# Kernel optimization log

Measured on AMD Instinct MI355X. Metric: run time of the kernel, lower is better.

Reference implementation:

```python
import jax, jax.numpy as jnp
import numpy as np

H = 10  # hidden_size


def _lstm_cell(x, h, c, Wih, Whh, bih, bhh):
    # PyTorch LSTMCell: gates ordered i, f, g, o
    gates = x @ Wih.T + bih + h @ Whh.T + bhh  # [B, 4H]
    i, f, g, o = jnp.split(gates, 4, axis=-1)
    c_new = jax.nn.sigmoid(f) * c + jax.nn.sigmoid(i) * jnp.tanh(g)
    h_new = jax.nn.sigmoid(o) * jnp.tanh(c_new)
    return h_new, c_new


def setup_inputs() -> dict:
    key = jax.random.key(0)
    ks = jax.random.split(key, 12)
    B, T = 16384, 2048
    s = 1.0 / np.sqrt(H)  # PyTorch LSTMCell init scale
    inp = {
        "x": jax.random.normal(ks[0], (B, T, 2), dtype=jnp.float32),
        "WihA": jax.random.uniform(ks[1], (4 * H, 2), minval=-s, maxval=s),
        "WhhA": jax.random.uniform(ks[2], (4 * H, H), minval=-s, maxval=s),
        "bihA": jax.random.uniform(ks[3], (4 * H,), minval=-s, maxval=s),
        "bhhA": jax.random.uniform(ks[4], (4 * H,), minval=-s, maxval=s),
        "WihB": jax.random.uniform(ks[5], (4 * H, 1), minval=-s, maxval=s),
        "WhhB": jax.random.uniform(ks[6], (4 * H, H), minval=-s, maxval=s),
        "bihB": jax.random.uniform(ks[7], (4 * H,), minval=-s, maxval=s),
        "bhhB": jax.random.uniform(ks[8], (4 * H,), minval=-s, maxval=s),
        "Wlin": jax.random.uniform(ks[9], (1, H), minval=-s, maxval=s),
        "blin": jax.random.uniform(ks[10], (1,), minval=-s, maxval=s),
    }
    return inp


def reference(x, WihA, WhhA, bihA, bhhA, WihB, WhhB, bihB, bhhB, Wlin, blin):
    B, T, _ = x.shape
    # time-major pairs: step 2k uses cellB on x[:, 2k, :1], step 2k+1 uses cellA on x[:, 2k+1, :]
    xs = jnp.transpose(x, (1, 0, 2)).reshape(T // 2, 2, B, 2)  # [T/2, 2, B, 2]
    h0 = jnp.zeros((B, H), dtype=x.dtype)
    c0 = jnp.zeros((B, H), dtype=x.dtype)

    def step(carry, x_pair):
        h, c = carry
        h, c = _lstm_cell(x_pair[0][:, :1], h, c, WihB, WhhB, bihB, bhhB)
        h, c = _lstm_cell(x_pair[1], h, c, WihA, WhhA, bihA, bhhA)
        return (h, c), None

    (h, c), _ = jax.lax.scan(step, (h0, c0), xs)
    # original stacks all hx but only uses the last timestep
    return jax.nn.sigmoid(h @ Wlin.T + blin)  # [B, 1]
```

## Files before the change

kernel.cpp:

```cpp
#include <hip/hip_runtime.h>
#include <math.h>

#define H 10
#define BATCH 16384
#define NPAIRS 1024
#define EPW 6
#define GSTRIDE 12

#define LOG2E 1.44269504088896340736f

#if __has_builtin(__builtin_amdgcn_exp2f)
#define EXP2(x) __builtin_amdgcn_exp2f(x)
#else
#define EXP2(x) exp2f(x)
#endif

typedef float v2f __attribute__((ext_vector_type(2)));

__device__ __forceinline__ float fast_rcp(float x) { return __builtin_amdgcn_rcpf(x); }

__device__ __forceinline__ v2f pk_mul(v2f a, v2f b) {
    v2f d;
    asm("v_pk_mul_f32 %0, %1, %2" : "=v"(d) : "v"(a), "v"(b));
    return d;
}
__device__ __forceinline__ v2f pk_fma(v2f a, v2f b, v2f c) {
    v2f d;
    asm("v_pk_fma_f32 %0, %1, %2, %3" : "=v"(d) : "v"(a), "v"(b), "v"(c));
    return d;
}

__global__ void __launch_bounds__(64) __attribute__((amdgpu_waves_per_eu(2, 3)))
lstm_kernel(const float* __restrict__ x,
            const float* __restrict__ WihA, const float* __restrict__ WhhA,
            const float* __restrict__ bihA, const float* __restrict__ bhhA,
            const float* __restrict__ WihB, const float* __restrict__ WhhB,
            const float* __restrict__ bihB, const float* __restrict__ bhhB,
            const float* __restrict__ Wlin, const float* __restrict__ blin,
            float* __restrict__ out)
{
    const int lane    = threadIdx.x;
    const int e_local = lane / H;
    const int j       = lane - e_local * H;
    const bool active = lane < EPW * H;
    const int elem    = blockIdx.x * EPW + e_local;
    const bool valid  = active && (elem < BATCH);
    const int jj      = active ? j : 0;
    const int elem_c  = valid ? elem : 0;

    __shared__ __align__(16) float hbuf[84];
    const int waddr = active ? (e_local * GSTRIDE + j) : (72 + (lane - 60));
    const int rbase = e_local * GSTRIDE;

    v2f wA2[4][5], wB2[4][5];
    float bA[4], bB[4], wxA0[4], wxA1[4], wxB[4];
#pragma unroll
    for (int g = 0; g < 4; ++g) {
        const float s = (g == 2) ? (2.0f * LOG2E) : (-LOG2E);
        const int row = g * H + jj;
        bA[g]   = s * (bihA[row] + bhhA[row]);
        bB[g]   = s * (bihB[row] + bhhB[row]);
        wxA0[g] = s * WihA[row * 2 + 0];
        wxA1[g] = s * WihA[row * 2 + 1];
        wxB[g]  = s * WihB[row];
#pragma unroll
        for (int m = 0; m < 5; ++m) {
            wA2[g][m] = (v2f){s * WhhA[row * H + 2 * m], s * WhhA[row * H + 2 * m + 1]};
            wB2[g][m] = (v2f){s * WhhB[row * H + 2 * m], s * WhhB[row * H + 2 * m + 1]};
        }
    }
#pragma unroll
    for (int g = 0; g < 4; ++g) {
        asm volatile("" : "+v"(bA[g]), "+v"(bB[g]), "+v"(wxA0[g]),
                          "+v"(wxA1[g]), "+v"(wxB[g]));
#pragma unroll
        for (int m = 0; m < 5; ++m) {
            asm volatile("" : "+v"(wA2[g][m]), "+v"(wB2[g][m]));
        }
    }

    const float4* __restrict__ xr = (const float4*)x + (size_t)elem_c * NPAIRS;

    float h = 0.0f, c = 0.0f;
    float4 xp = xr[0];

#pragma unroll 2
    for (int p = 0; p < NPAIRS; ++p) {
        const int pn = (p + 1 < NPAIRS) ? (p + 1) : p;
        const float4 xnext = xr[pn];

        {
            hbuf[waddr] = h;
            const float b0 = fmaf(wxB[0], xp.x, bB[0]);
            const float b1 = fmaf(wxB[1], xp.x, bB[1]);
            const float b2 = fmaf(wxB[2], xp.x, bB[2]);
            const float b3 = fmaf(wxB[3], xp.x, bB[3]);
            const float4 ha = *reinterpret_cast<const float4*>(&hbuf[rbase]);
            const float4 hb = *reinterpret_cast<const float4*>(&hbuf[rbase + 4]);
            const float2 hc = *reinterpret_cast<const float2*>(&hbuf[rbase + 8]);
            const v2f h01 = (v2f){ha.x, ha.y}, h23 = (v2f){ha.z, ha.w};
            const v2f h45 = (v2f){hb.x, hb.y}, h67 = (v2f){hb.z, hb.w};
            const v2f h89 = (v2f){hc.x, hc.y};

            v2f a0 = pk_mul(wB2[0][0], h01);
            v2f a1 = pk_mul(wB2[1][0], h01);
            v2f a2 = pk_mul(wB2[2][0], h01);
            v2f a3 = pk_mul(wB2[3][0], h01);
            a0 = pk_fma(wB2[0][1], h23, a0); a1 = pk_fma(wB2[1][1], h23, a1);
            a2 = pk_fma(wB2[2][1], h23, a2); a3 = pk_fma(wB2[3][1], h23, a3);
            a0 = pk_fma(wB2[0][2], h45, a0); a1 = pk_fma(wB2[1][2], h45, a1);
            a2 = pk_fma(wB2[2][2], h45, a2); a3 = pk_fma(wB2[3][2], h45, a3);
            a0 = pk_fma(wB2[0][3], h67, a0); a1 = pk_fma(wB2[1][3], h67, a1);
            a2 = pk_fma(wB2[2][3], h67, a2); a3 = pk_fma(wB2[3][3], h67, a3);
            a0 = pk_fma(wB2[0][4], h89, a0); a1 = pk_fma(wB2[1][4], h89, a1);
            a2 = pk_fma(wB2[2][4], h89, a2); a3 = pk_fma(wB2[3][4], h89, a3);

            const float y0 = (a0.x + a0.y) + b0;
            const float y1 = (a1.x + a1.y) + b1;
            const float y2 = (a2.x + a2.y) + b2;
            const float y3 = (a3.x + a3.y) + b3;

            const float ef = EXP2(y1);
            const float ei = EXP2(y0);
            const float eg = EXP2(-__builtin_fabsf(y2));
            const float eo = EXP2(y3);
            const float opf = 1.0f + ef;
            const float d1 = (1.0f + ei) * (1.0f + eg);
            const float tg = __builtin_copysignf((1.0f - eg) * opf, y2);
            const float num = fmaf(c, d1, tg);
            const float cn = num * fast_rcp(opf * d1);
            const float ec = EXP2((-2.0f * LOG2E) * __builtin_fabsf(cn));
            const float d2 = (1.0f + eo) * (1.0f + ec);
            h = __builtin_copysignf((1.0f - ec) * fast_rcp(d2), cn);
            c = cn;
        }

        {
            hbuf[waddr] = h;
            const float b0 = fmaf(wxA1[0], xp.w, fmaf(wxA0[0], xp.z, bA[0]));
            const float b1 = fmaf(wxA1[1], xp.w, fmaf(wxA0[1], xp.z, bA[1]));
            const float b2 = fmaf(wxA1[2], xp.w, fmaf(wxA0[2], xp.z, bA[2]));
            const float b3 = fmaf(wxA1[3], xp.w, fmaf(wxA0[3], xp.z, bA[3]));
            const float4 ha = *reinterpret_cast<const float4*>(&hbuf[rbase]);
            const float4 hb = *reinterpret_cast<const float4*>(&hbuf[rbase + 4]);
            const float2 hc = *reinterpret_cast<const float2*>(&hbuf[rbase + 8]);
            const v2f h01 = (v2f){ha.x, ha.y}, h23 = (v2f){ha.z, ha.w};
            const v2f h45 = (v2f){hb.x, hb.y}, h67 = (v2f){hb.z, hb.w};
            const v2f h89 = (v2f){hc.x, hc.y};

            v2f a0 = pk_mul(wA2[0][0], h01);
            v2f a1 = pk_mul(wA2[1][0], h01);
            v2f a2 = pk_mul(wA2[2][0], h01);
            v2f a3 = pk_mul(wA2[3][0], h01);
            a0 = pk_fma(wA2[0][1], h23, a0); a1 = pk_fma(wA2[1][1], h23, a1);
            a2 = pk_fma(wA2[2][1], h23, a2); a3 = pk_fma(wA2[3][1], h23, a3);
            a0 = pk_fma(wA2[0][2], h45, a0); a1 = pk_fma(wA2[1][2], h45, a1);
            a2 = pk_fma(wA2[2][2], h45, a2); a3 = pk_fma(wA2[3][2], h45, a3);
            a0 = pk_fma(wA2[0][3], h67, a0); a1 = pk_fma(wA2[1][3], h67, a1);
            a2 = pk_fma(wA2[2][3], h67, a2); a3 = pk_fma(wA2[3][3], h67, a3);
            a0 = pk_fma(wA2[0][4], h89, a0); a1 = pk_fma(wA2[1][4], h89, a1);
            a2 = pk_fma(wA2[2][4], h89, a2); a3 = pk_fma(wA2[3][4], h89, a3);

            const float y0 = (a0.x + a0.y) + b0;
            const float y1 = (a1.x + a1.y) + b1;
            const float y2 = (a2.x + a2.y) + b2;
            const float y3 = (a3.x + a3.y) + b3;

            const float ef = EXP2(y1);
            const float ei = EXP2(y0);
            const float eg = EXP2(-__builtin_fabsf(y2));
            const float eo = EXP2(y3);
            const float opf = 1.0f + ef;
            const float d1 = (1.0f + ei) * (1.0f + eg);
            const float tg = __builtin_copysignf((1.0f - eg) * opf, y2);
            const float num = fmaf(c, d1, tg);
            const float cn = num * fast_rcp(opf * d1);
            const float ec = EXP2((-2.0f * LOG2E) * __builtin_fabsf(cn));
            const float d2 = (1.0f + eo) * (1.0f + ec);
            h = __builtin_copysignf((1.0f - ec) * fast_rcp(d2), cn);
            c = cn;
        }

        xp = xnext;
    }

    {
        const float v = Wlin[jj] * h;
        hbuf[waddr] = v;
        const float4 ha = *reinterpret_cast<const float4*>(&hbuf[rbase]);
        const float4 hb = *reinterpret_cast<const float4*>(&hbuf[rbase + 4]);
        const float2 hc = *reinterpret_cast<const float2*>(&hbuf[rbase + 8]);
        const float s = ((ha.x + ha.y) + (ha.z + ha.w)) +
                        ((hb.x + hb.y) + (hb.z + hb.w)) + (hc.x + hc.y);
        if (valid && j == 0) {
            const float y = s + blin[0];
            out[elem] = fast_rcp(1.0f + EXP2(-LOG2E * y));
        }
    }
}

extern "C" void kernel_launch(void* const* d_in, const int* in_sizes, int n_in,
                              void* d_out, int out_size, void* d_ws, size_t ws_size,
                              hipStream_t stream) {
    const float* x    = (const float*)d_in[0];
    const float* WihA = (const float*)d_in[1];
    const float* WhhA = (const float*)d_in[2];
    const float* bihA = (const float*)d_in[3];
    const float* bhhA = (const float*)d_in[4];
    const float* WihB = (const float*)d_in[5];
    const float* WhhB = (const float*)d_in[6];
    const float* bihB = (const float*)d_in[7];
    const float* bhhB = (const float*)d_in[8];
    const float* Wlin = (const float*)d_in[9];
    const float* blin = (const float*)d_in[10];
    float* out = (float*)d_out;

    const int grid = (BATCH + EPW - 1) / EPW;
    hipLaunchKernelGGL(lstm_kernel, dim3(grid), dim3(64), 0, stream,
                       x, WihA, WhhA, bihA, bhhA, WihB, WhhB, bihB, bhhB,
                       Wlin, blin, out);
}
```

Baseline: 1.164 ms.

## Replace shared-memory hidden-state broadcast with ds_bpermute and deepen x prefetch

Each step previously broadcast h to all 10 lanes of an element by writing it to LDS and reading it back with three vector loads. It now uses ten ds_bpermute cross-lane reads, which removes the shared buffer and the write-then-read round trip. The change also prefetches x two pairs ahead instead of one, simplifies the g-gate tanh so it drops the abs and copysign, and removes the empty asm register pins on the weights. Ten bpermutes are more LDS-path instructions than one write plus three reads, and the simpler tanh can overflow for large inputs.

New measurement: 1.221 ms. 1.05x slower.

```diff
diff --git a/kernel.cpp b/kernel.cpp
--- a/kernel.cpp
+++ b/kernel.cpp
@@ -5,7 +5,6 @@
 #define BATCH 16384
 #define NPAIRS 1024
 #define EPW 6
-#define GSTRIDE 12
 
 #define LOG2E 1.44269504088896340736f
 
@@ -48,9 +47,7 @@
     const int jj      = active ? j : 0;
     const int elem_c  = valid ? elem : 0;
 
-    __shared__ __align__(16) float hbuf[84];
-    const int waddr = active ? (e_local * GSTRIDE + j) : (72 + (lane - 60));
-    const int rbase = e_local * GSTRIDE;
+    const int base4 = (e_local * H) << 2;
 
     v2f wA2[4][5], wB2[4][5];
     float bA[4], bB[4], wxA0[4], wxA1[4], wxB[4];
@@ -69,38 +66,37 @@
             wB2[g][m] = (v2f){s * WhhB[row * H + 2 * m], s * WhhB[row * H + 2 * m + 1]};
         }
     }
-#pragma unroll
-    for (int g = 0; g < 4; ++g) {
-        asm volatile("" : "+v"(bA[g]), "+v"(bB[g]), "+v"(wxA0[g]),
-                          "+v"(wxA1[g]), "+v"(wxB[g]));
-#pragma unroll
-        for (int m = 0; m < 5; ++m) {
-            asm volatile("" : "+v"(wA2[g][m]), "+v"(wB2[g][m]));
-        }
-    }
 
     const float4* __restrict__ xr = (const float4*)x + (size_t)elem_c * NPAIRS;
 
     float h = 0.0f, c = 0.0f;
     float4 xp = xr[0];
+    float4 xq = xr[1];
 
 #pragma unroll 2
     for (int p = 0; p < NPAIRS; ++p) {
-        const int pn = (p + 1 < NPAIRS) ? (p + 1) : p;
-        const float4 xnext = xr[pn];
+        const int pn2 = (p + 2 < NPAIRS) ? (p + 2) : (NPAIRS - 1);
+        const float4 xn = xr[pn2];
 
         {
-            hbuf[waddr] = h;
-            const float b0 = fmaf(wxB[0], xp.x, bB[0]);
-            const float b1 = fmaf(wxB[1], xp.x, bB[1]);
-            const float b2 = fmaf(wxB[2], xp.x, bB[2]);
-            const float b3 = fmaf(wxB[3], xp.x, bB[3]);
-            const float4 ha = *reinterpret_cast<const float4*>(&hbuf[rbase]);
-            const float4 hb = *reinterpret_cast<const float4*>(&hbuf[rbase + 4]);
-            const float2 hc = *reinterpret_cast<const float2*>(&hbuf[rbase + 8]);
-            const v2f h01 = (v2f){ha.x, ha.y}, h23 = (v2f){ha.z, ha.w};
-            const v2f h45 = (v2f){hb.x, hb.y}, h67 = (v2f){hb.z, hb.w};
-            const v2f h89 = (v2f){hc.x, hc.y};
+            float hk0 = __int_as_float(__builtin_amdgcn_ds_bpermute(base4 + 0,  __float_as_int(h)));
+            float hk1 = __int_as_float(__builtin_amdgcn_ds_bpermute(base4 + 4,  __float_as_int(h)));
+            float hk2 = __int_as_float(__builtin_amdgcn_ds_bpermute(base4 + 8,  __float_as_int(h)));
+            float hk3 = __int_as_float(__builtin_amdgcn_ds_bpermute(base4 + 12, __float_as_int(h)));
+            float hk4 = __int_as_float(__builtin_amdgcn_ds_bpermute(base4 + 16, __float_as_int(h)));
+            float hk5 = __int_as_float(__builtin_amdgcn_ds_bpermute(base4 + 20, __float_as_int(h)));
+            float hk6 = __int_as_float(__builtin_amdgcn_ds_bpermute(base4 + 24, __float_as_int(h)));
+            float hk7 = __int_as_float(__builtin_amdgcn_ds_bpermute(base4 + 28, __float_as_int(h)));
+            float hk8 = __int_as_float(__builtin_amdgcn_ds_bpermute(base4 + 32, __float_as_int(h)));
+            float hk9 = __int_as_float(__builtin_amdgcn_ds_bpermute(base4 + 36, __float_as_int(h)));
+            const v2f h01 = (v2f){hk0, hk1}, h23 = (v2f){hk2, hk3};
+            const v2f h45 = (v2f){hk4, hk5}, h67 = (v2f){hk6, hk7};
+            const v2f h89 = (v2f){hk8, hk9};
+
+            const float yb0 = fmaf(wxB[0], xp.x, bB[0]);
+            const float yb1 = fmaf(wxB[1], xp.x, bB[1]);
+            const float yb2 = fmaf(wxB[2], xp.x, bB[2]);
+            const float yb3 = fmaf(wxB[3], xp.x, bB[3]);
 
             v2f a0 = pk_mul(wB2[0][0], h01);
             v2f a1 = pk_mul(wB2[1][0], h01);
@@ -115,20 +111,19 @@
             a0 = pk_fma(wB2[0][4], h89, a0); a1 = pk_fma(wB2[1][4], h89, a1);
             a2 = pk_fma(wB2[2][4], h89, a2); a3 = pk_fma(wB2[3][4], h89, a3);
 
-            const float y0 = (a0.x + a0.y) + b0;
-            const float y1 = (a1.x + a1.y) + b1;
-            const float y2 = (a2.x + a2.y) + b2;
-            const float y3 = (a3.x + a3.y) + b3;
-
+            const float y0 = (a0.x + a0.y) + yb0;
+            const float y1 = (a1.x + a1.y) + yb1;
+            const float y2 = (a2.x + a2.y) + yb2;
+            const float y3 = (a3.x + a3.y) + yb3;
+
+            const float ei = EXP2(y0);
             const float ef = EXP2(y1);
-            const float ei = EXP2(y0);
-            const float eg = EXP2(-__builtin_fabsf(y2));
+            const float e2 = EXP2(y2);
             const float eo = EXP2(y3);
             const float opf = 1.0f + ef;
-            const float d1 = (1.0f + ei) * (1.0f + eg);
-            const float tg = __builtin_copysignf((1.0f - eg) * opf, y2);
-            const float num = fmaf(c, d1, tg);
-            const float cn = num * fast_rcp(opf * d1);
+            const float d1  = (1.0f + ei) * (1.0f + e2);
+            const float num = fmaf(c, d1, (e2 - 1.0f) * opf);
+            const float cn  = num * fast_rcp(opf * d1);
             const float ec = EXP2((-2.0f * LOG2E) * __builtin_fabsf(cn));
             const float d2 = (1.0f + eo) * (1.0f + ec);
             h = __builtin_copysignf((1.0f - ec) * fast_rcp(d2), cn);
@@ -136,17 +131,24 @@
         }
 
         {
-            hbuf[waddr] = h;
-            const float b0 = fmaf(wxA1[0], xp.w, fmaf(wxA0[0], xp.z, bA[0]));
-            const float b1 = fmaf(wxA1[1], xp.w, fmaf(wxA0[1], xp.z, bA[1]));
-            const float b2 = fmaf(wxA1[2], xp.w, fmaf(wxA0[2], xp.z, bA[2]));
-            const float b3 = fmaf(wxA1[3], xp.w, fmaf(wxA0[3], xp.z, bA[3]));
-            const float4 ha = *reinterpret_cast<const float4*>(&hbuf[rbase]);
-            const float4 hb = *reinterpret_cast<const float4*>(&hbuf[rbase + 4]);
-            const float2 hc = *reinterpret_cast<const float2*>(&hbuf[rbase + 8]);
-            const v2f h01 = (v2f){ha.x, ha.y}, h23 = (v2f){ha.z, ha.w};
-            const v2f h45 = (v2f){hb.x, hb.y}, h67 = (v2f){hb.z, hb.w};
-            const v2f h89 = (v2f){hc.x, hc.y};
+            float hk0 = __int_as_float(__builtin_amdgcn_ds_bpermute(base4 + 0,  __float_as_int(h)));
+            float hk1 = __int_as_float(__builtin_amdgcn_ds_bpermute(base4 + 4,  __float_as_int(h)));
+            float hk2 = __int_as_float(__builtin_amdgcn_ds_bpermute(base4 + 8,  __float_as_int(h)));
+            float hk3 = __int_as_float(__builtin_amdgcn_ds_bpermute(base4 + 12, __float_as_int(h)));
+            float hk4 = __int_as_float(__builtin_amdgcn_ds_bpermute(base4 + 16, __float_as_int(h)));
+            float hk5 = __int_as_float(__builtin_amdgcn_ds_bpermute(base4 + 20, __float_as_int(h)));
+            float hk6 = __int_as_float(__builtin_amdgcn_ds_bpermute(base4 + 24, __float_as_int(h)));
+            float hk7 = __int_as_float(__builtin_amdgcn_ds_bpermute(base4 + 28, __float_as_int(h)));
+            float hk8 = __int_as_float(__builtin_amdgcn_ds_bpermute(base4 + 32, __float_as_int(h)));
+            float hk9 = __int_as_float(__builtin_amdgcn_ds_bpermute(base4 + 36, __float_as_int(h)));
+            const v2f h01 = (v2f){hk0, hk1}, h23 = (v2f){hk2, hk3};
+            const v2f h45 = (v2f){hk4, hk5}, h67 = (v2f){hk6, hk7};
+            const v2f h89 = (v2f){hk8, hk9};
+
+            const float yb0 = fmaf(wxA1[0], xp.w, fmaf(wxA0[0], xp.z, bA[0]));
+            const float yb1 = fmaf(wxA1[1], xp.w, fmaf(wxA0[1], xp.z, bA[1]));
+            const float yb2 = fmaf(wxA1[2], xp.w, fmaf(wxA0[2], xp.z, bA[2]));
+            const float yb3 = fmaf(wxA1[3], xp.w, fmaf(wxA0[3], xp.z, bA[3]));
 
             v2f a0 = pk_mul(wA2[0][0], h01);
             v2f a1 = pk_mul(wA2[1][0], h01);
@@ -161,37 +163,37 @@
             a0 = pk_fma(wA2[0][4], h89, a0); a1 = pk_fma(wA2[1][4], h89, a1);
             a2 = pk_fma(wA2[2][4], h89, a2); a3 = pk_fma(wA2[3][4], h89, a3);
 
-            const float y0 = (a0.x + a0.y) + b0;
-            const float y1 = (a1.x + a1.y) + b1;
-            const float y2 = (a2.x + a2.y) + b2;
-            const float y3 = (a3.x + a3.y) + b3;
-
+            const float y0 = (a0.x + a0.y) + yb0;
+            const float y1 = (a1.x + a1.y) + yb1;
+            const float y2 = (a2.x + a2.y) + yb2;
+            const float y3 = (a3.x + a3.y) + yb3;
+
+            const float ei = EXP2(y0);
             const float ef = EXP2(y1);
-            const float ei = EXP2(y0);
-            const float eg = EXP2(-__builtin_fabsf(y2));
+            const float e2 = EXP2(y2);
             const float eo = EXP2(y3);
             const float opf = 1.0f + ef;
-            const float d1 = (1.0f + ei) * (1.0f + eg);
-            const float tg = __builtin_copysignf((1.0f - eg) * opf, y2);
-            const float num = fmaf(c, d1, tg);
-            const float cn = num * fast_rcp(opf * d1);
+            const float d1  = (1.0f + ei) * (1.0f + e2);
+            const float num = fmaf(c, d1, (e2 - 1.0f) * opf);
+            const float cn  = num * fast_rcp(opf * d1);
             const float ec = EXP2((-2.0f * LOG2E) * __builtin_fabsf(cn));
             const float d2 = (1.0f + eo) * (1.0f + ec);
             h = __builtin_copysignf((1.0f - ec) * fast_rcp(d2), cn);
             c = cn;
         }
 
-        xp = xnext;
+        xp = xq;
+        xq = xn;
     }
 
     {
         const float v = Wlin[jj] * h;
-        hbuf[waddr] = v;
-        const float4 ha = *reinterpret_cast<const float4*>(&hbuf[rbase]);
-        const float4 hb = *reinterpret_cast<const float4*>(&hbuf[rbase + 4]);
-        const float2 hc = *reinterpret_cast<const float2*>(&hbuf[rbase + 8]);
-        const float s = ((ha.x + ha.y) + (ha.z + ha.w)) +
-                        ((hb.x + hb.y) + (hb.z + hb.w)) + (hc.x + hc.y);
+        float s = v;
+#pragma unroll
+        for (int k = 1; k < H; ++k) {
+            s += __int_as_float(
+                __builtin_amdgcn_ds_bpermute(base4 + (k << 2), __float_as_int(v)));
+        }
         if (valid && j == 0) {
             const float y = s + blin[0];
             out[elem] = fast_rcp(1.0f + EXP2(-LOG2E * y));
```
